# Kernel tuning notes

Hardware: AMD Instinct MI355X
Metric: run time of the kernel (lower is better)

## Reference

```python
import jax, jax.numpy as jnp
import numpy as np

DIM, HEADS, KV_HEADS = 1024, 16, 4
B, T = 1, 4096
HEAD_DIM = DIM // HEADS           # 64
KV_DIM = DIM // (HEADS // KV_HEADS)  # 256
SCALE = HEAD_DIM ** -0.5


def setup_inputs() -> dict:
    key = jax.random.key(0)
    ks = jax.random.split(key, 9)
    s = lambda fan_in: fan_in ** -0.5
    return {
        "x": jax.random.normal(ks[0], (B, T, DIM), jnp.float32),
        "mask": jnp.tril(jnp.ones((1, 1, T, T), jnp.bool_)),  # causal
        "q_w": jax.random.normal(ks[1], (DIM, DIM), jnp.float32) * s(DIM),
        "q_b": jnp.zeros((DIM,), jnp.float32),
        "k_w": jax.random.normal(ks[2], (KV_DIM, DIM), jnp.float32) * s(DIM),
        "k_b": jnp.zeros((KV_DIM,), jnp.float32),
        "v_w": jax.random.normal(ks[3], (KV_DIM, DIM), jnp.float32) * s(DIM),
        "v_b": jnp.zeros((KV_DIM,), jnp.float32),
        "o_w": jax.random.normal(ks[4], (DIM, DIM), jnp.float32) * s(DIM),
        "o_b": jnp.zeros((DIM,), jnp.float32),
    }


def reference(x, mask, q_w, q_b, k_w, k_b, v_w, v_b, o_w, o_b):
    b, t, d = x.shape
    g = HEADS // KV_HEADS  # query heads per kv head
    # projections (torch Linear: x @ W^T + b)
    q = (x @ q_w.T + q_b).reshape(b, t, HEADS, HEAD_DIM).transpose(0, 2, 1, 3)      # [B,H,T,hd]
    k = (x @ k_w.T + k_b).reshape(b, t, KV_HEADS, HEAD_DIM).transpose(0, 2, 1, 3)   # [B,Hk,T,hd]
    v = (x @ v_w.T + v_b).reshape(b, t, KV_HEADS, HEAD_DIM).transpose(0, 2, 1, 3)   # [B,Hk,T,hd]
    # GQA: group query heads over shared kv heads
    qg = q.reshape(b, KV_HEADS, g, t, HEAD_DIM)                                     # [B,Hk,g,T,hd]
    scores = jnp.einsum('bkgtd,bksd->bkgts', qg, k) * SCALE                         # [B,Hk,g,T,T]
    scores = jnp.where(mask[:, :, None, :, :], scores, -1e9)
    attn = jax.nn.softmax(scores, axis=-1)  # dropout is identity in eval mode
    out = jnp.einsum('bkgts,bksd->bkgtd', attn, v)                                  # [B,Hk,g,T,hd]
    out = out.reshape(b, HEADS, t, HEAD_DIM).transpose(0, 2, 1, 3).reshape(b, t, d)
    out = out @ o_w.T + o_b
    return out, k, v  # (output, new kv cache)
```

## Files before the change

kernel.cpp:

```cpp
#include <hip/hip_runtime.h>
#include <hip/hip_bf16.h>
#include <stdint.h>

typedef __bf16 bf16;
typedef __bf16 bf16x8 __attribute__((ext_vector_type(8)));
typedef __bf16 bf16x4 __attribute__((ext_vector_type(4)));
typedef float  f32x4 __attribute__((ext_vector_type(4)));

#define SEQ   4096
#define DIM_  1024
#define HD_   64
#define NEG_BIG (-30000.0f)

#define QSCALE (0.125f * 1.4426950408889634f)

__device__ __forceinline__ bf16x8 cvt8(const float* p) {
    f32x4 a = *(const f32x4*)p, b = *(const f32x4*)(p + 4);
    bf16x8 r;
    r[0]=(bf16)a[0]; r[1]=(bf16)a[1]; r[2]=(bf16)a[2]; r[3]=(bf16)a[3];
    r[4]=(bf16)b[0]; r[5]=(bf16)b[1]; r[6]=(bf16)b[2]; r[7]=(bf16)b[3];
    return r;
}

__device__ __forceinline__ void gload16(const bf16* g, bf16* l) {
    __builtin_amdgcn_global_load_lds(
        (const __attribute__((address_space(1))) void*)g,
        (__attribute__((address_space(3))) void*)l, 16, 0, 0);
}

__global__ __launch_bounds__(256)
void conv_bf16(const float* __restrict__ x,  const float* __restrict__ qw,
               const float* __restrict__ kw, const float* __restrict__ vw,
               const float* __restrict__ ow,
               bf16* __restrict__ xb,  bf16* __restrict__ qwb,
               bf16* __restrict__ kwb, bf16* __restrict__ vwb,
               bf16* __restrict__ owb)
{
    int b = blockIdx.x;
    const float* s; bf16* d; int base;
    if (b < 2048)      { s = x;  d = xb;  base = b * 2048; }
    else if (b < 2560) { s = qw; d = qwb; base = (b - 2048) * 2048; }
    else if (b < 2688) { s = kw; d = kwb; base = (b - 2560) * 2048; }
    else if (b < 2816) { s = vw; d = vwb; base = (b - 2688) * 2048; }
    else               { s = ow; d = owb; base = (b - 2816) * 2048; }
    int i = base + threadIdx.x * 8;
    *(bf16x8*)(d + i) = cvt8(s + i);
}

template<int MODE, bool BWBF>
__global__ __launch_bounds__(256)
void gemm_bt(const bf16* __restrict__ A,
             const void* __restrict__ B0, const float* __restrict__ b0,
             const void* __restrict__ B1, const float* __restrict__ b1,
             const void* __restrict__ B2, const float* __restrict__ b2,
             float* __restrict__ C0, float* __restrict__ C1, float* __restrict__ C2,
             bf16* __restrict__ Qbf, bf16* __restrict__ Kbf, bf16* __restrict__ VTbf)
{
    const int K = 1024, NT = 32;
    const int tid  = threadIdx.x;
    const int lane = tid & 63, wave = tid >> 6;
    const int qd = lane >> 4, ln = lane & 15;
    const int wm = (wave & 1) * 32, wn = (wave >> 1) * 64;
    const int m0 = blockIdx.x * 64, n0 = blockIdx.y * 128;

    const void* Bp; const float* bias;
    if (MODE == 1) {
        if (n0 < 1024)      { Bp = (const bf16*)B0 + (size_t)n0 * K;        bias = b0 + n0; }
        else if (n0 < 1280) { Bp = (const bf16*)B1 + (size_t)(n0-1024) * K; bias = b1 + (n0-1024); }
        else                { Bp = (const bf16*)B2 + (size_t)(n0-1280) * K; bias = b2 + (n0-1280); }
    } else if (BWBF)        { Bp = (const bf16*)B0 + (size_t)n0 * K;        bias = b0 + n0; }
    else                    { Bp = (const float*)B0 + (size_t)n0 * K;       bias = b0 + n0; }

    __shared__ bf16 As[2][64*32];
    __shared__ bf16 Bs[2][128*32];

    const int gr = lane >> 2;
    const int gc = (((lane & 3) ^ ((gr >> 1) & 3))) * 8;
    const bf16* Ag  = A + (size_t)(m0 + wave*16 + gr) * K + gc;
    const bf16* Bg0 = (const bf16*)Bp + (size_t)(wave*32 + gr) * K + gc;
    const bf16* Bg1 = (const bf16*)Bp + (size_t)(wave*32 + 16 + gr) * K + gc;
    const int aW = (wave*16) * 32;
    const int bW0 = (wave*32) * 32, bW1 = (wave*32 + 16) * 32;

    const int sw = (qd ^ ((ln >> 1) & 3)) * 8;

    f32x4 acc[2][4] = {};

    if constexpr (MODE == 1 || BWBF) {
        auto stage = [&](int buf, int t) {
            int k0 = t * 32;
            gload16(Ag  + k0, &As[buf][aW]);
            gload16(Bg0 + k0, &Bs[buf][bW0]);
            gload16(Bg1 + k0, &Bs[buf][bW1]);
        };
        stage(0, 0);
        stage(1, 1);
        for (int t = 0; t < NT; ++t) {
            const int cur = t & 1;
            if (t < NT - 1) asm volatile("s_waitcnt vmcnt(3)" ::: "memory");
            else            asm volatile("s_waitcnt vmcnt(0)" ::: "memory");
            __builtin_amdgcn_s_barrier();

            bf16x8 af[2], bg[4];
            #pragma unroll
            for (int i = 0; i < 2; ++i)
                af[i] = *(const bf16x8*)(&As[cur][(wm + i*16 + ln)*32 + sw]);
            #pragma unroll
            for (int j = 0; j < 4; ++j)
                bg[j] = *(const bf16x8*)(&Bs[cur][(wn + j*16 + ln)*32 + sw]);
            #pragma unroll
            for (int i = 0; i < 2; ++i)
                #pragma unroll
                for (int j = 0; j < 4; ++j)
                    acc[i][j] = __builtin_amdgcn_mfma_f32_16x16x32_bf16(af[i], bg[j], acc[i][j], 0, 0, 0);

            if (t + 2 < NT) {
                __builtin_amdgcn_s_barrier();
                stage(cur, t + 2);
            }
        }
    } else {
        for (int t = 0; t < NT; ++t) {
            int k0 = t * 32;
            bf16x8 rb[2];
            #pragma unroll
            for (int i = 0; i < 2; ++i) {
                int s = i*256 + tid;
                int row = s >> 2, ch = s & 3;
                rb[i] = cvt8((const float*)Bp + (size_t)row*K + k0 + ch*8);
            }
            __syncthreads();
            gload16(Ag + k0, &As[0][aW]);
            #pragma unroll
            for (int i = 0; i < 2; ++i) {
                int s = i*256 + tid;
                int row = s >> 2, ch = s & 3;
                *(bf16x8*)(&Bs[0][row*32 + ((ch ^ ((row >> 1) & 3)) * 8)]) = rb[i];
            }
            __syncthreads();
            bf16x8 af[2], bg[4];
            #pragma unroll
            for (int i = 0; i < 2; ++i)
                af[i] = *(const bf16x8*)(&As[0][(wm + i*16 + ln)*32 + sw]);
            #pragma unroll
            for (int j = 0; j < 4; ++j)
                bg[j] = *(const bf16x8*)(&Bs[0][(wn + j*16 + ln)*32 + sw]);
            #pragma unroll
            for (int i = 0; i < 2; ++i)
                #pragma unroll
                for (int j = 0; j < 4; ++j)
                    acc[i][j] = __builtin_amdgcn_mfma_f32_16x16x32_bf16(af[i], bg[j], acc[i][j], 0, 0, 0);
        }
    }

    #pragma unroll
    for (int i = 0; i < 2; ++i) {
        #pragma unroll
        for (int j = 0; j < 4; ++j) {
            int colg = n0 + wn + j*16 + ln;
            float bv = bias[wn + j*16 + ln];
            if (MODE == 1 && colg >= 1280) {
                int c2 = colg - 1280;
                int rowg0 = m0 + wm + i*16 + qd*4;
                bf16x4 vt;
                #pragma unroll
                for (int r = 0; r < 4; ++r) {
                    float v = acc[i][j][r] + bv;
                    C2[(size_t)(c2 >> 6)*(SEQ*HD_) + (size_t)(rowg0 + r)*HD_ + (c2 & 63)] = v;
                    vt[r] = (bf16)v;
                }
                *(bf16x4*)(&VTbf[(size_t)(c2 >> 6)*(HD_*SEQ) + (size_t)(c2 & 63)*SEQ + rowg0]) = vt;
            } else {
                #pragma unroll
                for (int r = 0; r < 4; ++r) {
                    int rowg = m0 + wm + i*16 + qd*4 + r;
                    float v = acc[i][j][r] + bv;
                    if (MODE == 0) {
                        C0[(size_t)rowg*1024 + colg] = v;
                    } else if (colg < 1024) {
                        Qbf[(size_t)rowg*1024 + colg] = (bf16)(v * QSCALE);
                    } else {
                        int c2 = colg - 1024;
                        size_t idx = (size_t)(c2 >> 6)*(SEQ*HD_) + (size_t)rowg*HD_ + (c2 & 63);
                        C1[idx]  = v;
                        Kbf[idx] = (bf16)v;
                    }
                }
            }
        }
    }
}

__global__ __launch_bounds__(256)
void attn_fwd(const bf16* __restrict__ Q, const bf16* __restrict__ Kc,
              const bf16* __restrict__ VT, bf16* __restrict__ att)
{
    const int bid  = blockIdx.x;
    const int head = bid & 15;
    const int mt   = 63 - (bid >> 4);
    const int qb   = mt * 64;
    const int kvh  = head >> 2;

    const int tid = threadIdx.x, lane = tid & 63, wave = tid >> 6;
    const int qd = lane >> 4, ln = lane & 15;
    const int rw0 = qb + wave * 16;

    __shared__ bf16 Ks[64*72];
    __shared__ bf16 Vt[64*72];
    __shared__ bf16 Ps[4][16*72];
    __shared__ float Lr[4][16];

    const bf16* Kbase = Kc + (size_t)kvh * SEQ * HD_;
    const bf16* Vbase = VT + (size_t)kvh * HD_ * SEQ;

    bf16x8 aq[2];
    #pragma unroll
    for (int ks = 0; ks < 2; ++ks)
        aq[ks] = *(const bf16x8*)(Q + (size_t)(rw0 + ln)*DIM_ + head*HD_ + ks*32 + qd*8);

    f32x4 o[4] = {};
    float l_lane = 0.f;

    const float C16 = 16.0f * 1.4426950408889634f;
    const int nkt = mt + 1;

    const int r8a = tid >> 3,        cha = tid & 7;
    const int r8b = (256 + tid) >> 3, chb = tid & 7;

    bf16x8 rk[2], rv[2];
    rk[0] = *(const bf16x8*)(Kbase + (size_t)r8a*HD_ + cha*8);
    rv[0] = *(const bf16x8*)(Vbase + (size_t)r8a*SEQ + cha*8);
    rk[1] = *(const bf16x8*)(Kbase + (size_t)r8b*HD_ + chb*8);
    rv[1] = *(const bf16x8*)(Vbase + (size_t)r8b*SEQ + chb*8);

    for (int kt = 0; kt < nkt; ++kt) {
        const int kb = kt * 64;

        __syncthreads();
        *(bf16x8*)(Ks + r8a*72 + cha*8) = rk[0];
        *(bf16x8*)(Vt + r8a*72 + cha*8) = rv[0];
        *(bf16x8*)(Ks + r8b*72 + chb*8) = rk[1];
        *(bf16x8*)(Vt + r8b*72 + chb*8) = rv[1];

        if (kt + 1 < nkt) {
            rk[0] = *(const bf16x8*)(Kbase + (size_t)(kb + 64 + r8a)*HD_ + cha*8);
            rv[0] = *(const bf16x8*)(Vbase + (size_t)r8a*SEQ + kb + 64 + cha*8);
            rk[1] = *(const bf16x8*)(Kbase + (size_t)(kb + 64 + r8b)*HD_ + chb*8);
            rv[1] = *(const bf16x8*)(Vbase + (size_t)r8b*SEQ + kb + 64 + chb*8);
        }
        asm volatile("s_waitcnt lgkmcnt(0)" ::: "memory");
        __builtin_amdgcn_s_barrier();

        f32x4 S[4] = {};
        #pragma unroll
        for (int ks = 0; ks < 2; ++ks) {
            bf16x8 bk[4];
            #pragma unroll
            for (int nf = 0; nf < 4; ++nf)
                bk[nf] = *(const bf16x8*)(Ks + (nf*16 + ln)*72 + ks*32 + qd*8);
            #pragma unroll
            for (int nf = 0; nf < 4; ++nf)
                S[nf] = __builtin_amdgcn_mfma_f32_16x16x32_bf16(bk[nf], aq[ks], S[nf], 0, 0, 0);
        }

        if (kt == nkt - 1) {
            int qrow = rw0 + ln;
            #pragma unroll
            for (int nf = 0; nf < 4; ++nf) {
                #pragma unroll
                for (int r = 0; r < 4; ++r) {
                    int kcol = kb + nf*16 + qd*4 + r;
                    if (kcol > qrow) S[nf][r] = NEG_BIG;
                }
            }
        }

        bf16* Pw = &Ps[wave][0];
        #pragma unroll
        for (int nf = 0; nf < 4; ++nf) {
            bf16x4 pk;
            #pragma unroll
            for (int r = 0; r < 4; ++r) {
                float p = exp2f(S[nf][r] - C16);
                l_lane += p;
                pk[r] = (bf16)p;
            }
            *(bf16x4*)(Pw + ln*72 + nf*16 + qd*4) = pk;
        }
        asm volatile("s_waitcnt lgkmcnt(0)" ::: "memory");

        #pragma unroll
        for (int ks = 0; ks < 2; ++ks) {
            bf16x8 bv[4];
            #pragma unroll
            for (int nf = 0; nf < 4; ++nf)
                bv[nf] = *(const bf16x8*)(Vt + (nf*16 + ln)*72 + ks*32 + qd*8);
            bf16x8 ap = *(const bf16x8*)(&Ps[wave][ln*72 + ks*32 + qd*8]);
            #pragma unroll
            for (int nf = 0; nf < 4; ++nf)
                o[nf] = __builtin_amdgcn_mfma_f32_16x16x32_bf16(ap, bv[nf], o[nf], 0, 0, 0);
        }
    }

    l_lane += __shfl_xor(l_lane, 16);
    l_lane += __shfl_xor(l_lane, 32);
    Lr[wave][ln] = l_lane;
    asm volatile("s_waitcnt lgkmcnt(0)" ::: "memory");
    #pragma unroll
    for (int r = 0; r < 4; ++r) {
        float inv = 1.0f / Lr[wave][qd*4 + r];
        int trow = rw0 + qd*4 + r;
        #pragma unroll
        for (int nf = 0; nf < 4; ++nf)
            att[(size_t)trow*DIM_ + head*HD_ + nf*16 + ln] = (bf16)(o[nf][r] * inv);
    }
}

extern "C" void kernel_launch(void* const* d_in, const int* in_sizes, int n_in,
                              void* d_out, int out_size, void* d_ws, size_t ws_size,
                              hipStream_t stream)
{
    const float* x  = (const float*)d_in[0];
    const float* qw = (const float*)d_in[2];
    const float* qb = (const float*)d_in[3];
    const float* kw = (const float*)d_in[4];
    const float* kb = (const float*)d_in[5];
    const float* vw = (const float*)d_in[6];
    const float* vb = (const float*)d_in[7];
    const float* ow = (const float*)d_in[8];
    const float* ob = (const float*)d_in[9];

    float* out  = (float*)d_out;
    float* kout = out  + (size_t)SEQ * DIM_;
    float* vout = kout + (size_t)4 * SEQ * HD_;

    bf16* q_bf  = (bf16*)d_out;
    bf16* k_bf  = q_bf  + (size_t)SEQ * DIM_;
    bf16* vT_bf = k_bf  + (size_t)4 * SEQ * HD_;
    bf16* qw_bf = vT_bf + (size_t)4 * HD_ * SEQ;
    bf16* kw_bf = qw_bf + (size_t)1024 * 1024;
    bf16* vw_bf = kw_bf + (size_t)256 * 1024;

    bf16* x_bf = (bf16*)d_ws;
    bf16* att  = (bf16*)d_ws;
    bool  owbf_ok = ws_size >= (size_t)(8*1024*1024 + 2*1024*1024);
    bf16* ow_bf = owbf_ok ? (bf16*)((char*)d_ws + (size_t)8*1024*1024) : nullptr;

    int convBlocks = 2816 + (owbf_ok ? 512 : 0);
    conv_bf16<<<convBlocks, 256, 0, stream>>>(x, qw, kw, vw, ow,
                                              x_bf, qw_bf, kw_bf, vw_bf, ow_bf);

    gemm_bt<1, true><<<dim3(64, 12), 256, 0, stream>>>(x_bf, qw_bf, qb, kw_bf, kb, vw_bf, vb,
                                                       nullptr, kout, vout,
                                                       q_bf, k_bf, vT_bf);
    attn_fwd<<<dim3(1024), 256, 0, stream>>>(q_bf, k_bf, vT_bf, att);
    if (owbf_ok)
        gemm_bt<0, true><<<dim3(64, 8), 256, 0, stream>>>(att, ow_bf, ob, nullptr, nullptr,
                                                          nullptr, nullptr, out, nullptr, nullptr,
                                                          nullptr, nullptr, nullptr);
    else
        gemm_bt<0, false><<<dim3(64, 8), 256, 0, stream>>>(att, ow, ob, nullptr, nullptr,
                                                           nullptr, nullptr, out, nullptr, nullptr,
                                                           nullptr, nullptr, nullptr);
}
```

Baseline: 237.9 us.

## Double GEMM K-tile to 64 with XOR swizzle; raise wave priority around attention MFMAs

The projection GEMMs now stage 64-wide K tiles, so there are half as many barrier-separated iterations. Each stage issues more 16-byte loads per wave and uses an 8-way XOR swizzle to avoid LDS bank conflicts. The attention kernel wraps its QK and PV MFMA blocks in s_setprio so waves in matrix phases get scheduling priority over the others. In exchange, LDS use doubles, which may reduce occupancy, and the fp32-weight fallback path holds more registers.

```diff
diff --git a/kernel.cpp b/kernel.cpp
--- a/kernel.cpp
+++ b/kernel.cpp
@@ -56,7 +56,7 @@
              float* __restrict__ C0, float* __restrict__ C1, float* __restrict__ C2,
              bf16* __restrict__ Qbf, bf16* __restrict__ Kbf, bf16* __restrict__ VTbf)
 {
-    const int K = 1024, NT = 32;
+    const int K = 1024, NT = 16;
     const int tid  = threadIdx.x;
     const int lane = tid & 63, wave = tid >> 6;
     const int qd = lane >> 4, ln = lane & 15;
@@ -71,48 +71,50 @@
     } else if (BWBF)        { Bp = (const bf16*)B0 + (size_t)n0 * K;        bias = b0 + n0; }
     else                    { Bp = (const float*)B0 + (size_t)n0 * K;       bias = b0 + n0; }
 
-    __shared__ bf16 As[2][64*32];
-    __shared__ bf16 Bs[2][128*32];
-
-    const int gr = lane >> 2;
-    const int gc = (((lane & 3) ^ ((gr >> 1) & 3))) * 8;
-    const bf16* Ag  = A + (size_t)(m0 + wave*16 + gr) * K + gc;
-    const bf16* Bg0 = (const bf16*)Bp + (size_t)(wave*32 + gr) * K + gc;
-    const bf16* Bg1 = (const bf16*)Bp + (size_t)(wave*32 + 16 + gr) * K + gc;
-    const int aW = (wave*16) * 32;
-    const int bW0 = (wave*32) * 32, bW1 = (wave*32 + 16) * 32;
-
-    const int sw = (qd ^ ((ln >> 1) & 3)) * 8;
+    __shared__ bf16 As[2][64*64];
+    __shared__ bf16 Bs[2][128*64];
+
+    const int gr8 = lane >> 3;
+    const int gcol = ((lane & 7) ^ (gr8 & 7)) * 8;
+    const bf16* AgB = A + (size_t)(m0 + wave*16 + gr8) * K + gcol;
+    const bf16* BgB = (const bf16*)Bp + (size_t)(wave*32 + gr8) * K + gcol;
 
     f32x4 acc[2][4] = {};
 
     if constexpr (MODE == 1 || BWBF) {
         auto stage = [&](int buf, int t) {
-            int k0 = t * 32;
-            gload16(Ag  + k0, &As[buf][aW]);
-            gload16(Bg0 + k0, &Bs[buf][bW0]);
-            gload16(Bg1 + k0, &Bs[buf][bW1]);
+            int k0 = t * 64;
+            #pragma unroll
+            for (int i = 0; i < 2; ++i)
+                gload16(AgB + (size_t)(i*8)*K + k0, &As[buf][(wave*16 + i*8)*64]);
+            #pragma unroll
+            for (int i = 0; i < 4; ++i)
+                gload16(BgB + (size_t)(i*8)*K + k0, &Bs[buf][(wave*32 + i*8)*64]);
         };
         stage(0, 0);
         stage(1, 1);
         for (int t = 0; t < NT; ++t) {
             const int cur = t & 1;
-            if (t < NT - 1) asm volatile("s_waitcnt vmcnt(3)" ::: "memory");
+            if (t < NT - 1) asm volatile("s_waitcnt vmcnt(6)" ::: "memory");
             else            asm volatile("s_waitcnt vmcnt(0)" ::: "memory");
             __builtin_amdgcn_s_barrier();
 
-            bf16x8 af[2], bg[4];
-            #pragma unroll
-            for (int i = 0; i < 2; ++i)
-                af[i] = *(const bf16x8*)(&As[cur][(wm + i*16 + ln)*32 + sw]);
-            #pragma unroll
-            for (int j = 0; j < 4; ++j)
-                bg[j] = *(const bf16x8*)(&Bs[cur][(wn + j*16 + ln)*32 + sw]);
-            #pragma unroll
-            for (int i = 0; i < 2; ++i)
+            #pragma unroll
+            for (int ks = 0; ks < 2; ++ks) {
+                const int sw = ((ks*4 + qd) ^ (ln & 7)) * 8;
+                bf16x8 af[2], bg[4];
+                #pragma unroll
+                for (int i = 0; i < 2; ++i)
+                    af[i] = *(const bf16x8*)(&As[cur][(wm + i*16 + ln)*64 + sw]);
                 #pragma unroll
                 for (int j = 0; j < 4; ++j)
-                    acc[i][j] = __builtin_amdgcn_mfma_f32_16x16x32_bf16(af[i], bg[j], acc[i][j], 0, 0, 0);
+                    bg[j] = *(const bf16x8*)(&Bs[cur][(wn + j*16 + ln)*64 + sw]);
+                #pragma unroll
+                for (int i = 0; i < 2; ++i)
+                    #pragma unroll
+                    for (int j = 0; j < 4; ++j)
+                        acc[i][j] = __builtin_amdgcn_mfma_f32_16x16x32_bf16(af[i], bg[j], acc[i][j], 0, 0, 0);
+            }
 
             if (t + 2 < NT) {
                 __builtin_amdgcn_s_barrier();
@@ -121,35 +123,41 @@
         }
     } else {
         for (int t = 0; t < NT; ++t) {
-            int k0 = t * 32;
-            bf16x8 rb[2];
-            #pragma unroll
-            for (int i = 0; i < 2; ++i) {
-                int s = i*256 + tid;
-                int row = s >> 2, ch = s & 3;
-                rb[i] = cvt8((const float*)Bp + (size_t)row*K + k0 + ch*8);
+            int k0 = t * 64;
+            bf16x8 rb[4];
+            #pragma unroll
+            for (int i = 0; i < 4; ++i) {
+                int c = i*256 + tid;
+                int row = c >> 3, ch = c & 7;
+                rb[i] = cvt8((const float*)Bp + (size_t)row*K + k0 + ((ch ^ (row & 7)) * 8));
             }
             __syncthreads();
-            gload16(Ag + k0, &As[0][aW]);
-            #pragma unroll
-            for (int i = 0; i < 2; ++i) {
-                int s = i*256 + tid;
-                int row = s >> 2, ch = s & 3;
-                *(bf16x8*)(&Bs[0][row*32 + ((ch ^ ((row >> 1) & 3)) * 8)]) = rb[i];
+            #pragma unroll
+            for (int i = 0; i < 2; ++i)
+                gload16(AgB + (size_t)(i*8)*K + k0, &As[0][(wave*16 + i*8)*64]);
+            #pragma unroll
+            for (int i = 0; i < 4; ++i) {
+                int c = i*256 + tid;
+                int row = c >> 3, ch = c & 7;
+                *(bf16x8*)(&Bs[0][row*64 + ch*8]) = rb[i];
             }
             __syncthreads();
-            bf16x8 af[2], bg[4];
-            #pragma unroll
-            for (int i = 0; i < 2; ++i)
-                af[i] = *(const bf16x8*)(&As[0][(wm + i*16 + ln)*32 + sw]);
-            #pragma unroll
-            for (int j = 0; j < 4; ++j)
-                bg[j] = *(const bf16x8*)(&Bs[0][(wn + j*16 + ln)*32 + sw]);
-            #pragma unroll
-            for (int i = 0; i < 2; ++i)
+            #pragma unroll
+            for (int ks = 0; ks < 2; ++ks) {
+                const int sw = ((ks*4 + qd) ^ (ln & 7)) * 8;
+                bf16x8 af[2], bg[4];
+                #pragma unroll
+                for (int i = 0; i < 2; ++i)
+                    af[i] = *(const bf16x8*)(&As[0][(wm + i*16 + ln)*64 + sw]);
                 #pragma unroll
                 for (int j = 0; j < 4; ++j)
-                    acc[i][j] = __builtin_amdgcn_mfma_f32_16x16x32_bf16(af[i], bg[j], acc[i][j], 0, 0, 0);
+                    bg[j] = *(const bf16x8*)(&Bs[0][(wn + j*16 + ln)*64 + sw]);
+                #pragma unroll
+                for (int i = 0; i < 2; ++i)
+                    #pragma unroll
+                    for (int j = 0; j < 4; ++j)
+                        acc[i][j] = __builtin_amdgcn_mfma_f32_16x16x32_bf16(af[i], bg[j], acc[i][j], 0, 0, 0);
+            }
         }
     }
 
@@ -252,6 +260,7 @@
         __builtin_amdgcn_s_barrier();
 
         f32x4 S[4] = {};
+        __builtin_amdgcn_s_setprio(1);
         #pragma unroll
         for (int ks = 0; ks < 2; ++ks) {
             bf16x8 bk[4];
@@ -262,6 +271,7 @@
             for (int nf = 0; nf < 4; ++nf)
                 S[nf] = __builtin_amdgcn_mfma_f32_16x16x32_bf16(bk[nf], aq[ks], S[nf], 0, 0, 0);
         }
+        __builtin_amdgcn_s_setprio(0);
 
         if (kt == nkt - 1) {
             int qrow = rw0 + ln;
@@ -289,6 +299,7 @@
         }
         asm volatile("s_waitcnt lgkmcnt(0)" ::: "memory");
 
+        __builtin_amdgcn_s_setprio(1);
         #pragma unroll
         for (int ks = 0; ks < 2; ++ks) {
             bf16x8 bv[4];
@@ -300,6 +311,7 @@
             for (int nf = 0; nf < 4; ++nf)
                 o[nf] = __builtin_amdgcn_mfma_f32_16x16x32_bf16(ap, bv[nf], o[nf], 0, 0, 0);
         }
+        __builtin_amdgcn_s_setprio(0);
     }
 
     l_lane += __shfl_xor(l_lane, 16);
```

Result: no change. 233.8 us (-1.7%).
